# Optimization experiments

Hardware: AMD Instinct MI355X
Metric: run time of the kernel (lower is better)

The kernel has to match this reference:

```python
import jax, jax.numpy as jnp
import numpy as np

N = 131072      # total nodes (1024 graphs x 128 nodes)
E = 1048576     # edges (avg degree 8)
IN = 74         # atom feature length
H = 128         # dim_embedding == all hidden_feats
B = 1024        # batch_size (graphs)
L = 3           # number of GCN+GRU layers


def setup_inputs() -> dict:
    key = jax.random.key(0)
    ks = jax.random.split(key, 10)
    node_feats = jax.random.normal(ks[0], (N, IN), dtype=jnp.float32)
    src = jax.random.randint(ks[1], (E,), 0, N, dtype=jnp.int32)
    dst = jax.random.randint(ks[2], (E,), 0, N, dtype=jnp.int32)
    s_in = 1.0 / np.sqrt(IN)
    s_h = 1.0 / np.sqrt(H)
    # init_transform: Linear(IN, H, bias=False); padding=True zeros the last output unit
    W_init = jax.random.normal(ks[3], (IN, H), dtype=jnp.float32) * s_in
    W_init = W_init.at[:, -1].set(0.0)
    lin_W = jax.random.normal(ks[4], (L, H, H), dtype=jnp.float32) * s_h
    lin_b = jax.random.normal(ks[5], (L, H), dtype=jnp.float32) * s_h
    gru_Wih = jax.random.normal(ks[6], (L, 3 * H, H), dtype=jnp.float32) * s_h
    gru_Whh = jax.random.normal(ks[7], (L, 3 * H, H), dtype=jnp.float32) * s_h
    gru_bih = jax.random.normal(ks[8], (L, 3 * H), dtype=jnp.float32) * s_h
    gru_bhh = jax.random.normal(ks[9], (L, 3 * H), dtype=jnp.float32) * s_h
    return {
        "node_feats": node_feats, "src": src, "dst": dst,
        "W_init": W_init, "lin_W": lin_W, "lin_b": lin_b,
        "gru_Wih": gru_Wih, "gru_Whh": gru_Whh,
        "gru_bih": gru_bih, "gru_bhh": gru_bhh,
        "batch_size": B,
    }


def _gru_cell(x, h, Wih, Whh, bih, bhh):
    # PyTorch GRUCell semantics
    gi = x @ Wih.T + bih   # [N, 3H]
    gh = h @ Whh.T + bhh   # [N, 3H]
    i_r, i_z, i_n = jnp.split(gi, 3, axis=-1)
    h_r, h_z, h_n = jnp.split(gh, 3, axis=-1)
    r = jax.nn.sigmoid(i_r + h_r)
    z = jax.nn.sigmoid(i_z + h_z)
    n = jnp.tanh(i_n + r * h_n)
    return (1.0 - z) * n + z * h


def reference(node_feats, src, dst, W_init, lin_W, lin_b,
              gru_Wih, gru_Whh, gru_bih, gru_bhh, batch_size):
    n_nodes = node_feats.shape[0]
    h = node_feats @ W_init  # init_transform (no bias)
    for l in range(lin_W.shape[0]):
        # update_all: sum incoming source features (scatter-add over edges)
        agg = jax.ops.segment_sum(h[src], dst, num_segments=n_nodes)
        x = jax.nn.relu(agg @ lin_W[l].T + lin_b[l])
        h = _gru_cell(x, h, gru_Wih[l], gru_Whh[l], gru_bih[l], gru_bhh[l])
    return h.reshape(batch_size, -1, h.shape[-1])
```

## Files before the change

### kernel.cpp

```cpp
#include <hip/hip_runtime.h>
#include <hip/hip_bf16.h>

#define NN 131072
#define EE 1048576
#define IN_F 74
#define HH 128
#define LL 3

using f32x4  = __attribute__((ext_vector_type(4))) float;
using f32x16 = __attribute__((ext_vector_type(16))) float;
using bf16x8 = __attribute__((ext_vector_type(8))) short;
typedef unsigned short ushort_t;
typedef unsigned int uint_t;

__device__ __forceinline__ short f2bf(float f) {
    __hip_bfloat16 b = __float2bfloat16(f);
    return __builtin_bit_cast(short, b);
}
__device__ __forceinline__ float bf2f(short s) {
    unsigned int u = ((unsigned int)(unsigned short)s) << 16;
    return __builtin_bit_cast(float, u);
}
__device__ __forceinline__ float bitf(uint_t u) { return __builtin_bit_cast(float, u); }
__device__ __forceinline__ float sigmoidf_(float x) { return 1.f / (1.f + __expf(-x)); }
__device__ __forceinline__ float tanhf_(float x)
{
    x = fminf(fmaxf(x, -15.f), 15.f);
    float e2 = __expf(2.f * x);
    return (e2 - 1.f) / (e2 + 1.f);
}

__global__ __launch_bounds__(256) void k_init_gemm(
    const float* __restrict__ nf, const float* __restrict__ Wi,
    ushort_t* __restrict__ hhi, ushort_t* __restrict__ hlo)
{
    __shared__ float Wis[IN_F * HH];
    __shared__ float nfs[32 * IN_F];
    int b = blockIdx.x;
    int t = threadIdx.x;

    for (int i = t; i < IN_F * HH / 4; i += 256)
        reinterpret_cast<float4*>(Wis)[i] = reinterpret_cast<const float4*>(Wi)[i];
    {
        const float4* nf4 = reinterpret_cast<const float4*>(nf + (long)b * 32 * IN_F);
        for (int i = t; i < 32 * IN_F / 4; i += 256)
            reinterpret_cast<float4*>(nfs)[i] = nf4[i];
    }
    __syncthreads();

    int nl = t >> 3;
    int c0 = (t & 7) * 4;
    float acc[4][4];
#pragma unroll
    for (int hf = 0; hf < 4; ++hf)
#pragma unroll
        for (int j = 0; j < 4; ++j) acc[hf][j] = 0.f;

    const float* nrow = nfs + nl * IN_F;
#pragma unroll 2
    for (int k = 0; k < IN_F; ++k) {
        float a = nrow[k];
#pragma unroll
        for (int hf = 0; hf < 4; ++hf) {
            float4 wv = *reinterpret_cast<const float4*>(Wis + k * HH + hf * 32 + c0);
            acc[hf][0] += a * wv.x;
            acc[hf][1] += a * wv.y;
            acc[hf][2] += a * wv.z;
            acc[hf][3] += a * wv.w;
        }
    }

    int node = b * 32 + nl;
#pragma unroll
    for (int hf = 0; hf < 4; ++hf) {
        uint_t uh[2], ul[2];
#pragma unroll
        for (int p = 0; p < 2; ++p) {
            float v0 = acc[hf][p * 2], v1 = acc[hf][p * 2 + 1];
            short h0 = f2bf(v0), h1 = f2bf(v1);
            short l0 = f2bf(v0 - bf2f(h0)), l1 = f2bf(v1 - bf2f(h1));
            uh[p] = (uint_t)(ushort_t)h0 | ((uint_t)(ushort_t)h1 << 16);
            ul[p] = (uint_t)(ushort_t)l0 | ((uint_t)(ushort_t)l1 << 16);
        }
        long adr = (long)node * HH + hf * 32 + c0;
        *reinterpret_cast<uint2*>(hhi + adr) = make_uint2(uh[0], uh[1]);
        *reinterpret_cast<uint2*>(hlo + adr) = make_uint2(ul[0], ul[1]);
    }
}

__global__ __launch_bounds__(256) void k_hist(const int* __restrict__ dsti, int* __restrict__ deg)
{
    int e = blockIdx.x * 256 + threadIdx.x;
    atomicAdd(&deg[dsti[e]], 1);
}

__global__ __launch_bounds__(256) void k_scan1(const int* __restrict__ deg, int* __restrict__ bsum)
{
    __shared__ int s[256];
    int b = blockIdx.x, t = threadIdx.x;
    int v = 0;
#pragma unroll
    for (int i = 0; i < 4; ++i) v += deg[b * 1024 + t * 4 + i];
    s[t] = v;
    __syncthreads();
    for (int st = 128; st > 0; st >>= 1) {
        if (t < st) s[t] += s[t + st];
        __syncthreads();
    }
    if (t == 0) bsum[b] = s[0];
}

__global__ void k_scan2(int* __restrict__ bsum, int nb)
{
    if (threadIdx.x == 0) {
        int run = 0;
        for (int i = 0; i < nb; ++i) { int v = bsum[i]; bsum[i] = run; run += v; }
    }
}

__global__ __launch_bounds__(256) void k_scan3(
    const int* __restrict__ deg, const int* __restrict__ bsum, int* __restrict__ row_start)
{
    __shared__ int s[256];
    int b = blockIdx.x, t = threadIdx.x;
    int base = b * 1024 + t * 4;
    int d0 = deg[base], d1 = deg[base + 1], d2 = deg[base + 2], d3 = deg[base + 3];
    int local = d0 + d1 + d2 + d3;
    s[t] = local;
    __syncthreads();
    for (int st = 1; st < 256; st <<= 1) {
        int v = (t >= st) ? s[t - st] : 0;
        __syncthreads();
        s[t] += v;
        __syncthreads();
    }
    int excl = s[t] - local + bsum[b];
    row_start[base] = excl;
    row_start[base + 1] = excl + d0;
    row_start[base + 2] = excl + d0 + d1;
    row_start[base + 3] = excl + d0 + d1 + d2;
    if (b == gridDim.x - 1 && t == 255) row_start[NN] = excl + local;
}

__global__ __launch_bounds__(256) void k_fill(
    const int* __restrict__ src, const int* __restrict__ dsti,
    const int* __restrict__ row_start, int* __restrict__ cursor, int* __restrict__ csr_src)
{
    int e = blockIdx.x * 256 + threadIdx.x;
    int d = dsti[e];
    int pos = atomicAdd(&cursor[d], 1);
    csr_src[row_start[d] + pos] = src[e];
}

__global__ __launch_bounds__(256) void k_split(
    const float* __restrict__ srcw, ushort_t* __restrict__ hi,
    ushort_t* __restrict__ lo, int n)
{
    int i = blockIdx.x * 256 + threadIdx.x;
    if (i >= n) return;
    float a = srcw[i];
    short h = f2bf(a);
    float rem = a - bf2f(h);
    hi[i] = (ushort_t)h;
    lo[i] = (ushort_t)f2bf(rem);
}

#define EIDX_CAP 1024

template <bool LDSIDX>
__device__ __forceinline__ void gather_node(
    const ushort_t* __restrict__ plane, const int* __restrict__ eidx,
    const int* __restrict__ csr_src, int estart, int e0, int e1, int c4,
    float& a0, float& a1, float& a2, float& a3)
{
    int e = e0;
    for (; e + 7 < e1; e += 8) {
        uint2 v[8];
#pragma unroll
        for (int u = 0; u < 8; ++u) {
            int s = LDSIDX ? eidx[e + u] : csr_src[estart + e + u];
            v[u] = *reinterpret_cast<const uint2*>(plane + (long)s * HH + c4);
        }
#pragma unroll
        for (int u = 0; u < 8; ++u) {
            a0 += bitf(v[u].x << 16);
            a1 += bitf(v[u].x & 0xffff0000u);
            a2 += bitf(v[u].y << 16);
            a3 += bitf(v[u].y & 0xffff0000u);
        }
    }
    for (; e < e1; ++e) {
        int s = LDSIDX ? eidx[e] : csr_src[estart + e];
        uint2 vv = *reinterpret_cast<const uint2*>(plane + (long)s * HH + c4);
        a0 += bitf(vv.x << 16);
        a1 += bitf(vv.x & 0xffff0000u);
        a2 += bitf(vv.y << 16);
        a3 += bitf(vv.y & 0xffff0000u);
    }
}

__global__ __launch_bounds__(256) void k_x(
    const ushort_t* __restrict__ hhi, const ushort_t* __restrict__ hlo,
    const int* __restrict__ row_start, const int* __restrict__ csr_src,
    const ushort_t* __restrict__ lWhi, const ushort_t* __restrict__ lWlo,
    const float* __restrict__ lb,
    ushort_t* __restrict__ xhi, ushort_t* __restrict__ xlo)
{
    __shared__ float aggs[32 * 128];
    __shared__ int eidx[EIDX_CAP];
    char* abase = (char*)aggs;
    int n0 = blockIdx.x * 32;
    int t = threadIdx.x;
    int w = t >> 6, lane = t & 63;

    int estart = row_start[n0];
    int ecount = row_start[n0 + 32] - estart;
    bool inl = (ecount <= EIDX_CAP);
    for (int i = t; i < ecount && i < EIDX_CAP; i += 256)
        eidx[i] = csr_src[estart + i];
    __syncthreads();

    const ushort_t* plane = (lane >= 32) ? hlo : hhi;
    int c4 = (lane & 31) * 4;

    for (int i = 0; i < 8; ++i) {
        int nl = w * 8 + i;
        int node = n0 + nl;
        int e0 = row_start[node] - estart;
        int e1 = row_start[node + 1] - estart;
        float a0 = 0.f, a1 = 0.f, a2 = 0.f, a3 = 0.f;
        if (inl)
            gather_node<true>(plane, eidx, csr_src, estart, e0, e1, c4, a0, a1, a2, a3);
        else
            gather_node<false>(plane, eidx, csr_src, estart, e0, e1, c4, a0, a1, a2, a3);
        a0 += __shfl_xor(a0, 32, 64);
        a1 += __shfl_xor(a1, 32, 64);
        a2 += __shfl_xor(a2, 32, 64);
        a3 += __shfl_xor(a3, 32, 64);
        if (lane < 32) {
            int swz = (nl & 7) << 4;
            float4 st = make_float4(a0, a1, a2, a3);
            *reinterpret_cast<float4*>(abase + ((nl * 512 + c4 * 4) ^ swz)) = st;
        }
    }
    __syncthreads();

    int ng = w >> 1, jg = w & 1;
    int l16 = lane & 15, lq = lane >> 4;

    f32x4 acc[4];
#pragma unroll
    for (int js = 0; js < 4; ++js) acc[js] = (f32x4){0.f, 0.f, 0.f, 0.f};

#pragma unroll
    for (int kk = 0; kk < 4; ++kk) {
        int k0 = kk * 32;
        int nodeL = ng * 16 + l16;
        int kb = (k0 + lq * 8) * 4;
        int swz = (nodeL & 7) << 4;
        float4 f0 = *reinterpret_cast<const float4*>(abase + ((nodeL * 512 + kb) ^ swz));
        float4 f1 = *reinterpret_cast<const float4*>(abase + ((nodeL * 512 + kb + 16) ^ swz));
        float av[8] = {f0.x, f0.y, f0.z, f0.w, f1.x, f1.y, f1.z, f1.w};
        bf16x8 ahi, alo;
#pragma unroll
        for (int e = 0; e < 8; ++e) {
            short hh_ = f2bf(av[e]);
            ahi[e] = hh_;
            alo[e] = f2bf(av[e] - bf2f(hh_));
        }
#pragma unroll
        for (int js = 0; js < 4; ++js) {
            int jrow = jg * 64 + js * 16 + l16;
            bf16x8 Bh = *reinterpret_cast<const bf16x8*>(lWhi + (long)jrow * HH + k0 + lq * 8);
            bf16x8 Bl = *reinterpret_cast<const bf16x8*>(lWlo + (long)jrow * HH + k0 + lq * 8);
            acc[js] = __builtin_amdgcn_mfma_f32_16x16x32_bf16(ahi, Bh, acc[js], 0, 0, 0);
            acc[js] = __builtin_amdgcn_mfma_f32_16x16x32_bf16(ahi, Bl, acc[js], 0, 0, 0);
            acc[js] = __builtin_amdgcn_mfma_f32_16x16x32_bf16(alo, Bh, acc[js], 0, 0, 0);
        }
    }

#pragma unroll
    for (int js = 0; js < 4; ++js) {
        int j = jg * 64 + js * 16 + l16;
        float bj = lb[j];
#pragma unroll
        for (int r = 0; r < 4; ++r) {
            int node = n0 + ng * 16 + lq * 4 + r;
            float v = fmaxf(acc[js][r] + bj, 0.f);
            long adr = (long)node * HH + j;
            short hi_ = f2bf(v);
            xhi[adr] = (ushort_t)hi_;
            xlo[adr] = (ushort_t)f2bf(v - bf2f(hi_));
        }
    }
}

#define LDSA(p) ((p) * 16384)
#define LDSB(p) (65536 + (p) * 32768)

__device__ __forceinline__ void stage_slab(
    const ushort_t* __restrict__ g, char* lds, int tid, int nchunk512)
{
    const uint4* g4 = reinterpret_cast<const uint4*>(g);
#pragma unroll
    for (int i = 0; i < 4; ++i) {
        if (i >= nchunk512) break;
        int c = i * 512 + tid;
        int L = c * 16;
        int row = L >> 8, kb = L & 255;
        *reinterpret_cast<uint4*>(lds + row * 256 + (kb ^ ((row & 15) << 4))) = g4[c];
    }
}

__device__ __forceinline__ void gru_half(
    f32x16& acc, const char* smem, int pAhi, int myoff, int rs_my,
    int jjoff, int rs_jj, int lh)
{
    bf16x8 Ahi[8], Alo[8];
#pragma unroll
    for (int kc = 0; kc < 8; ++kc) {
        int kb = kc * 32 + lh * 16;
        Ahi[kc] = *reinterpret_cast<const bf16x8*>(smem + LDSA(pAhi)     + myoff + (kb ^ rs_my));
        Alo[kc] = *reinterpret_cast<const bf16x8*>(smem + LDSA(pAhi + 1) + myoff + (kb ^ rs_my));
    }
#pragma unroll
    for (int kc = 0; kc < 8; ++kc) {
        int kb = kc * 32 + lh * 16;
        bf16x8 wh = *reinterpret_cast<const bf16x8*>(smem + LDSB(0) + jjoff + (kb ^ rs_jj));
        bf16x8 wl = *reinterpret_cast<const bf16x8*>(smem + LDSB(1) + jjoff + (kb ^ rs_jj));
        acc = __builtin_amdgcn_mfma_f32_32x32x16_bf16(Ahi[kc], wh, acc, 0, 0, 0);
        acc = __builtin_amdgcn_mfma_f32_32x32x16_bf16(Ahi[kc], wl, acc, 0, 0, 0);
        acc = __builtin_amdgcn_mfma_f32_32x32x16_bf16(Alo[kc], wh, acc, 0, 0, 0);
    }
}

__global__ void k_gru(
    const ushort_t* __restrict__ xhi, const ushort_t* __restrict__ xlo,
    ushort_t* __restrict__ hhi, ushort_t* __restrict__ hlo,
    const ushort_t* __restrict__ Wihhi, const ushort_t* __restrict__ Wihlo,
    const ushort_t* __restrict__ Whhhi, const ushort_t* __restrict__ Whhlo,
    const float* __restrict__ bi, const float* __restrict__ bh)
{
    __shared__ uint4 smem4[131072 / 16];
    char* smem = (char*)smem4;

    int t = threadIdx.x;
    int w = t >> 6, lane = t & 63;
    int ng = w >> 2, og = w & 3;
    int l31 = lane & 31, lh = lane >> 5;
    int n0 = blockIdx.x * 64;
    int myrow = ng * 32 + l31;
    int jj = og * 32 + l31;
    int myoff = myrow * 256, rs_my = (myrow & 15) << 4;
    int jjoff = jj * 256,   rs_jj = (jj & 15) << 4;

    stage_slab(xhi + (long)n0 * HH, smem + LDSA(0), t, 2);
    stage_slab(xlo + (long)n0 * HH, smem + LDSA(1), t, 2);
    stage_slab(hhi + (long)n0 * HH, smem + LDSA(2), t, 2);
    stage_slab(hlo + (long)n0 * HH, smem + LDSA(3), t, 2);
    stage_slab(Whhhi + 256 * HH, smem + LDSB(0), t, 4);
    stage_slab(Whhlo + 256 * HH, smem + LDSB(1), t, 4);
    __syncthreads();

    f32x16 acc1;
#pragma unroll
    for (int i = 0; i < 16; ++i) acc1[i] = 0.f;
    gru_half(acc1, smem, 2, myoff, rs_my, jjoff, rs_jj, lh);

    f32x16 acc2;
#pragma unroll
    for (int i = 0; i < 16; ++i) acc2[i] = 0.f;
    __syncthreads();
    stage_slab(Wihhi, smem + LDSB(0), t, 4);
    stage_slab(Wihlo, smem + LDSB(1), t, 4);
    __syncthreads();
    gru_half(acc2, smem, 0, myoff, rs_my, jjoff, rs_jj, lh);
    __syncthreads();
    stage_slab(Whhhi, smem + LDSB(0), t, 4);
    stage_slab(Whhlo, smem + LDSB(1), t, 4);
    __syncthreads();
    gru_half(acc2, smem, 2, myoff, rs_my, jjoff, rs_jj, lh);
    {
        float bR = bi[jj] + bh[jj];
        float bNh = bh[256 + jj];
#pragma unroll
        for (int i = 0; i < 16; ++i)
            acc1[i] = sigmoidf_(acc2[i] + bR) * (acc1[i] + bNh);
    }

#pragma unroll
    for (int i = 0; i < 16; ++i) acc2[i] = 0.f;
    __syncthreads();
    stage_slab(Wihhi + 256 * HH, smem + LDSB(0), t, 4);
    stage_slab(Wihlo + 256 * HH, smem + LDSB(1), t, 4);
    __syncthreads();
    gru_half(acc2, smem, 0, myoff, rs_my, jjoff, rs_jj, lh);
    {
        float bNi = bi[256 + jj];
#pragma unroll
        for (int i = 0; i < 16; ++i)
            acc1[i] = tanhf_(acc2[i] + bNi + acc1[i]);
    }

#pragma unroll
    for (int i = 0; i < 16; ++i) acc2[i] = 0.f;
    __syncthreads();
    stage_slab(Wihhi + 128 * HH, smem + LDSB(0), t, 4);
    stage_slab(Wihlo + 128 * HH, smem + LDSB(1), t, 4);
    __syncthreads();
    gru_half(acc2, smem, 0, myoff, rs_my, jjoff, rs_jj, lh);
    __syncthreads();
    stage_slab(Whhhi + 128 * HH, smem + LDSB(0), t, 4);
    stage_slab(Whhlo + 128 * HH, smem + LDSB(1), t, 4);
    __syncthreads();
    gru_half(acc2, smem, 2, myoff, rs_my, jjoff, rs_jj, lh);

    {
        float bZ = bi[128 + jj] + bh[128 + jj];
        int kb2 = 2 * jj;
#pragma unroll
        for (int reg = 0; reg < 16; ++reg) {
            int ndl = ng * 32 + (reg & 3) + 8 * (reg >> 2) + 4 * lh;
            long adr = (long)(n0 + ndl) * HH + jj;
            int rsn = (ndl & 15) << 4;
            float hold = bf2f(*reinterpret_cast<const short*>(smem + LDSA(2) + ndl * 256 + (kb2 ^ rsn)))
                       + bf2f(*reinterpret_cast<const short*>(smem + LDSA(3) + ndl * 256 + (kb2 ^ rsn)));
            float zv = sigmoidf_(acc2[reg] + bZ);
            float hp = (1.f - zv) * acc1[reg] + zv * hold;
            short hi_ = f2bf(hp);
            hhi[adr] = (ushort_t)hi_;
            hlo[adr] = (ushort_t)f2bf(hp - bf2f(hi_));
        }
    }
}

__global__ __launch_bounds__(256) void k_copy(
    const uint_t* __restrict__ hhi, const uint_t* __restrict__ hlo,
    float2* __restrict__ out)
{
    long i = (long)blockIdx.x * 256 + threadIdx.x;
    uint_t vh = hhi[i], vl = hlo[i];
    float2 o;
    o.x = bitf(vh << 16) + bitf(vl << 16);
    o.y = bitf(vh & 0xffff0000u) + bitf(vl & 0xffff0000u);
    out[i] = o;
}

extern "C" void kernel_launch(void* const* d_in, const int* in_sizes, int n_in,
                              void* d_out, int out_size, void* d_ws, size_t ws_size,
                              hipStream_t stream)
{
    const float* nf     = (const float*)d_in[0];
    const int*   src    = (const int*)d_in[1];
    const int*   dsti   = (const int*)d_in[2];
    const float* W_init = (const float*)d_in[3];
    const float* lin_W  = (const float*)d_in[4];
    const float* lin_b  = (const float*)d_in[5];
    const float* Wih    = (const float*)d_in[6];
    const float* Whh    = (const float*)d_in[7];
    const float* bih    = (const float*)d_in[8];
    const float* bhh    = (const float*)d_in[9];

    char* ws = (char*)d_ws;
    ushort_t* hhi = (ushort_t*)ws;
    ushort_t* hlo = (ushort_t*)(ws + (32ull << 20));
    ushort_t* xhi = (ushort_t*)(ws + (64ull << 20));
    ushort_t* xlo = (ushort_t*)(ws + (96ull << 20));
    int* deg    = (int*)(ws + (64ull << 20));
    int* cursor = (int*)(ws + (64ull << 20) + (1 << 20));
    int* bsum   = (int*)(ws + (64ull << 20) + (2 << 20));

    char* ob = (char*)d_out;
    int* row_start = (int*)ob;
    int* csr_src   = (int*)(ob + (1ull << 20));
    ushort_t* lWhi  = (ushort_t*)(ob + (6ull << 20));
    ushort_t* lWlo  = lWhi  + 3 * 128 * 128;
    ushort_t* Wihhi = lWlo  + 3 * 128 * 128;
    ushort_t* Wihlo = Wihhi + 3 * 384 * 128;
    ushort_t* Whhhi = Wihlo + 3 * 384 * 128;
    ushort_t* Whhlo = Whhhi + 3 * 384 * 128;

    k_init_gemm<<<NN / 32, 256, 0, stream>>>(nf, W_init, hhi, hlo);

    hipMemsetAsync(deg, 0, (size_t)NN * 4, stream);
    hipMemsetAsync(cursor, 0, (size_t)NN * 4, stream);
    k_hist<<<EE / 256, 256, 0, stream>>>(dsti, deg);
    k_scan1<<<NN / 1024, 256, 0, stream>>>(deg, bsum);
    k_scan2<<<1, 64, 0, stream>>>(bsum, NN / 1024);
    k_scan3<<<NN / 1024, 256, 0, stream>>>(deg, bsum, row_start);
    k_fill<<<EE / 256, 256, 0, stream>>>(src, dsti, row_start, cursor, csr_src);

    k_split<<<(3 * 128 * 128 + 255) / 256, 256, 0, stream>>>(lin_W, lWhi, lWlo, 3 * 128 * 128);
    k_split<<<(3 * 384 * 128 + 255) / 256, 256, 0, stream>>>(Wih, Wihhi, Wihlo, 3 * 384 * 128);
    k_split<<<(3 * 384 * 128 + 255) / 256, 256, 0, stream>>>(Whh, Whhhi, Whhlo, 3 * 384 * 128);

    for (int l = 0; l < LL; ++l) {
        k_x<<<NN / 32, 256, 0, stream>>>(
            hhi, hlo, row_start, csr_src,
            lWhi + (long)l * 128 * 128, lWlo + (long)l * 128 * 128,
            lin_b + (long)l * 128, xhi, xlo);
        k_gru<<<NN / 64, 512, 0, stream>>>(
            xhi, xlo, hhi, hlo,
            Wihhi + (long)l * 384 * 128, Wihlo + (long)l * 384 * 128,
            Whhhi + (long)l * 384 * 128, Whhlo + (long)l * 384 * 128,
            bih + (long)l * 384, bhh + (long)l * 384);
    }

    k_copy<<<NN * HH / 2 / 256, 256, 0, stream>>>((const uint_t*)hhi, (const uint_t*)hlo, (float2*)d_out);
}
```

Baseline: 972.9 us.

## Interleave h hi/lo planes per node and double-buffer GRU weight slabs

The hidden state is stored as one interleaved buffer (hi and lo bf16 halves adjacent per node), so each gathered source row is a single contiguous 512-byte read instead of two separate 256-byte reads from distinct planes. The GRU kernel is restructured into a 12-step loop over weight slabs that stages hi and lo weights separately into alternating LDS buffers, prefetching the next slab into registers while the current one is consumed. This replaces the serial stage/sync/compute pattern and cuts the LDS weight footprint per step. It adds register pressure for the prefetch and keeps two barriers per step.

```diff
diff --git a/kernel.cpp b/kernel.cpp
--- a/kernel.cpp
+++ b/kernel.cpp
@@ -32,7 +32,7 @@
 
 __global__ __launch_bounds__(256) void k_init_gemm(
     const float* __restrict__ nf, const float* __restrict__ Wi,
-    ushort_t* __restrict__ hhi, ushort_t* __restrict__ hlo)
+    ushort_t* __restrict__ h2)
 {
     __shared__ float Wis[IN_F * HH];
     __shared__ float nfs[32 * IN_F];
@@ -82,9 +82,9 @@
             uh[p] = (uint_t)(ushort_t)h0 | ((uint_t)(ushort_t)h1 << 16);
             ul[p] = (uint_t)(ushort_t)l0 | ((uint_t)(ushort_t)l1 << 16);
         }
-        long adr = (long)node * HH + hf * 32 + c0;
-        *reinterpret_cast<uint2*>(hhi + adr) = make_uint2(uh[0], uh[1]);
-        *reinterpret_cast<uint2*>(hlo + adr) = make_uint2(ul[0], ul[1]);
+        long adr = (long)node * 256 + hf * 32 + c0;
+        *reinterpret_cast<uint2*>(h2 + adr) = make_uint2(uh[0], uh[1]);
+        *reinterpret_cast<uint2*>(h2 + adr + 128) = make_uint2(ul[0], ul[1]);
     }
 }
 
@@ -169,8 +169,8 @@
 
 template <bool LDSIDX>
 __device__ __forceinline__ void gather_node(
-    const ushort_t* __restrict__ plane, const int* __restrict__ eidx,
-    const int* __restrict__ csr_src, int estart, int e0, int e1, int c4,
+    const ushort_t* __restrict__ h2, const int* __restrict__ eidx,
+    const int* __restrict__ csr_src, int estart, int e0, int e1, int l4,
     float& a0, float& a1, float& a2, float& a3)
 {
     int e = e0;
@@ -179,7 +179,7 @@
 #pragma unroll
         for (int u = 0; u < 8; ++u) {
             int s = LDSIDX ? eidx[e + u] : csr_src[estart + e + u];
-            v[u] = *reinterpret_cast<const uint2*>(plane + (long)s * HH + c4);
+            v[u] = *reinterpret_cast<const uint2*>(h2 + (long)s * 256 + l4);
         }
 #pragma unroll
         for (int u = 0; u < 8; ++u) {
@@ -191,7 +191,7 @@
     }
     for (; e < e1; ++e) {
         int s = LDSIDX ? eidx[e] : csr_src[estart + e];
-        uint2 vv = *reinterpret_cast<const uint2*>(plane + (long)s * HH + c4);
+        uint2 vv = *reinterpret_cast<const uint2*>(h2 + (long)s * 256 + l4);
         a0 += bitf(vv.x << 16);
         a1 += bitf(vv.x & 0xffff0000u);
         a2 += bitf(vv.y << 16);
@@ -200,7 +200,7 @@
 }
 
 __global__ __launch_bounds__(256) void k_x(
-    const ushort_t* __restrict__ hhi, const ushort_t* __restrict__ hlo,
+    const ushort_t* __restrict__ h2,
     const int* __restrict__ row_start, const int* __restrict__ csr_src,
     const ushort_t* __restrict__ lWhi, const ushort_t* __restrict__ lWlo,
     const float* __restrict__ lb,
@@ -220,8 +220,7 @@
         eidx[i] = csr_src[estart + i];
     __syncthreads();
 
-    const ushort_t* plane = (lane >= 32) ? hlo : hhi;
-    int c4 = (lane & 31) * 4;
+    int l4 = lane * 4;
 
     for (int i = 0; i < 8; ++i) {
         int nl = w * 8 + i;
@@ -230,9 +229,9 @@
         int e1 = row_start[node + 1] - estart;
         float a0 = 0.f, a1 = 0.f, a2 = 0.f, a3 = 0.f;
         if (inl)
-            gather_node<true>(plane, eidx, csr_src, estart, e0, e1, c4, a0, a1, a2, a3);
+            gather_node<true>(h2, eidx, csr_src, estart, e0, e1, l4, a0, a1, a2, a3);
         else
-            gather_node<false>(plane, eidx, csr_src, estart, e0, e1, c4, a0, a1, a2, a3);
+            gather_node<false>(h2, eidx, csr_src, estart, e0, e1, l4, a0, a1, a2, a3);
         a0 += __shfl_xor(a0, 32, 64);
         a1 += __shfl_xor(a1, 32, 64);
         a2 += __shfl_xor(a2, 32, 64);
@@ -240,7 +239,7 @@
         if (lane < 32) {
             int swz = (nl & 7) << 4;
             float4 st = make_float4(a0, a1, a2, a3);
-            *reinterpret_cast<float4*>(abase + ((nl * 512 + c4 * 4) ^ swz)) = st;
+            *reinterpret_cast<float4*>(abase + ((nl * 512 + l4 * 4) ^ swz)) = st;
         }
     }
     __syncthreads();
@@ -295,125 +294,138 @@
     }
 }
 
-#define LDSA(p) ((p) * 16384)
-#define LDSB(p) (65536 + (p) * 32768)
-
-__device__ __forceinline__ void stage_slab(
-    const ushort_t* __restrict__ g, char* lds, int tid, int nchunk512)
-{
-    const uint4* g4 = reinterpret_cast<const uint4*>(g);
-#pragma unroll
-    for (int i = 0; i < 4; ++i) {
-        if (i >= nchunk512) break;
-        int c = i * 512 + tid;
-        int L = c * 16;
-        int row = L >> 8, kb = L & 255;
-        *reinterpret_cast<uint4*>(lds + row * 256 + (kb ^ ((row & 15) << 4))) = g4[c];
-    }
-}
-
-__device__ __forceinline__ void gru_half(
-    f32x16& acc, const char* smem, int pAhi, int myoff, int rs_my,
-    int jjoff, int rs_jj, int lh)
-{
-    bf16x8 Ahi[8], Alo[8];
+#define LDS_XH 0
+#define LDS_XL 16384
+#define LDS_H2 32768
+#define LDS_B0 65536
+#define LDS_B1 98304
+
+__device__ __forceinline__ void slab_mfma(
+    f32x16& acc, const char* pAhi, const char* pAlo, int rs_my,
+    const char* pB, int rs_jj, int lh, bool twoM)
+{
 #pragma unroll
     for (int kc = 0; kc < 8; ++kc) {
         int kb = kc * 32 + lh * 16;
-        Ahi[kc] = *reinterpret_cast<const bf16x8*>(smem + LDSA(pAhi)     + myoff + (kb ^ rs_my));
-        Alo[kc] = *reinterpret_cast<const bf16x8*>(smem + LDSA(pAhi + 1) + myoff + (kb ^ rs_my));
-    }
-#pragma unroll
-    for (int kc = 0; kc < 8; ++kc) {
-        int kb = kc * 32 + lh * 16;
-        bf16x8 wh = *reinterpret_cast<const bf16x8*>(smem + LDSB(0) + jjoff + (kb ^ rs_jj));
-        bf16x8 wl = *reinterpret_cast<const bf16x8*>(smem + LDSB(1) + jjoff + (kb ^ rs_jj));
-        acc = __builtin_amdgcn_mfma_f32_32x32x16_bf16(Ahi[kc], wh, acc, 0, 0, 0);
-        acc = __builtin_amdgcn_mfma_f32_32x32x16_bf16(Ahi[kc], wl, acc, 0, 0, 0);
-        acc = __builtin_amdgcn_mfma_f32_32x32x16_bf16(Alo[kc], wh, acc, 0, 0, 0);
+        bf16x8 a0 = *reinterpret_cast<const bf16x8*>(pAhi + (kb ^ rs_my));
+        bf16x8 bb = *reinterpret_cast<const bf16x8*>(pB + (kb ^ rs_jj));
+        acc = __builtin_amdgcn_mfma_f32_32x32x16_bf16(a0, bb, acc, 0, 0, 0);
+        if (twoM) {
+            bf16x8 a1 = *reinterpret_cast<const bf16x8*>(pAlo + (kb ^ rs_my));
+            acc = __builtin_amdgcn_mfma_f32_32x32x16_bf16(a1, bb, acc, 0, 0, 0);
+        }
     }
 }
 
 __global__ void k_gru(
     const ushort_t* __restrict__ xhi, const ushort_t* __restrict__ xlo,
-    ushort_t* __restrict__ hhi, ushort_t* __restrict__ hlo,
+    ushort_t* __restrict__ h2,
     const ushort_t* __restrict__ Wihhi, const ushort_t* __restrict__ Wihlo,
     const ushort_t* __restrict__ Whhhi, const ushort_t* __restrict__ Whhlo,
     const float* __restrict__ bi, const float* __restrict__ bh)
 {
     __shared__ uint4 smem4[131072 / 16];
     char* smem = (char*)smem4;
-
     int t = threadIdx.x;
     int w = t >> 6, lane = t & 63;
     int ng = w >> 2, og = w & 3;
     int l31 = lane & 31, lh = lane >> 5;
     int n0 = blockIdx.x * 64;
-    int myrow = ng * 32 + l31;
-    int jj = og * 32 + l31;
-    int myoff = myrow * 256, rs_my = (myrow & 15) << 4;
-    int jjoff = jj * 256,   rs_jj = (jj & 15) << 4;
-
-    stage_slab(xhi + (long)n0 * HH, smem + LDSA(0), t, 2);
-    stage_slab(xlo + (long)n0 * HH, smem + LDSA(1), t, 2);
-    stage_slab(hhi + (long)n0 * HH, smem + LDSA(2), t, 2);
-    stage_slab(hlo + (long)n0 * HH, smem + LDSA(3), t, 2);
-    stage_slab(Whhhi + 256 * HH, smem + LDSB(0), t, 4);
-    stage_slab(Whhlo + 256 * HH, smem + LDSB(1), t, 4);
-    __syncthreads();
-
-    f32x16 acc1;
-#pragma unroll
-    for (int i = 0; i < 16; ++i) acc1[i] = 0.f;
-    gru_half(acc1, smem, 2, myoff, rs_my, jjoff, rs_jj, lh);
-
-    f32x16 acc2;
-#pragma unroll
-    for (int i = 0; i < 16; ++i) acc2[i] = 0.f;
-    __syncthreads();
-    stage_slab(Wihhi, smem + LDSB(0), t, 4);
-    stage_slab(Wihlo, smem + LDSB(1), t, 4);
-    __syncthreads();
-    gru_half(acc2, smem, 0, myoff, rs_my, jjoff, rs_jj, lh);
-    __syncthreads();
-    stage_slab(Whhhi, smem + LDSB(0), t, 4);
-    stage_slab(Whhlo, smem + LDSB(1), t, 4);
-    __syncthreads();
-    gru_half(acc2, smem, 2, myoff, rs_my, jjoff, rs_jj, lh);
+    int myrow = ng * 32 + l31, jj = og * 32 + l31;
+    int rs_my = (myrow & 15) << 4, rs_jj = (jj & 15) << 4;
+
+    const ushort_t* wsrc[12] = {
+        Whhhi + 256 * HH, Whhlo + 256 * HH,
+        Wihhi,            Wihlo,
+        Whhhi,            Whhlo,
+        Wihhi + 256 * HH, Wihlo + 256 * HH,
+        Wihhi + 128 * HH, Wihlo + 128 * HH,
+        Whhhi + 128 * HH, Whhlo + 128 * HH };
+    const bool aH[12] = {1, 1, 0, 0, 1, 1, 0, 0, 0, 0, 1, 1};
+
+    uint4 p0, p1, p2, p3;
     {
-        float bR = bi[jj] + bh[jj];
-        float bNh = bh[256 + jj];
-#pragma unroll
-        for (int i = 0; i < 16; ++i)
-            acc1[i] = sigmoidf_(acc2[i] + bR) * (acc1[i] + bNh);
-    }
-
-#pragma unroll
-    for (int i = 0; i < 16; ++i) acc2[i] = 0.f;
-    __syncthreads();
-    stage_slab(Wihhi + 256 * HH, smem + LDSB(0), t, 4);
-    stage_slab(Wihlo + 256 * HH, smem + LDSB(1), t, 4);
-    __syncthreads();
-    gru_half(acc2, smem, 0, myoff, rs_my, jjoff, rs_jj, lh);
+        const uint4* g = reinterpret_cast<const uint4*>(wsrc[0]);
+        p0 = g[t]; p1 = g[512 + t]; p2 = g[1024 + t]; p3 = g[1536 + t];
+    }
     {
-        float bNi = bi[256 + jj];
-#pragma unroll
-        for (int i = 0; i < 16; ++i)
-            acc1[i] = tanhf_(acc2[i] + bNi + acc1[i]);
-    }
-
-#pragma unroll
-    for (int i = 0; i < 16; ++i) acc2[i] = 0.f;
-    __syncthreads();
-    stage_slab(Wihhi + 128 * HH, smem + LDSB(0), t, 4);
-    stage_slab(Wihlo + 128 * HH, smem + LDSB(1), t, 4);
-    __syncthreads();
-    gru_half(acc2, smem, 0, myoff, rs_my, jjoff, rs_jj, lh);
-    __syncthreads();
-    stage_slab(Whhhi + 128 * HH, smem + LDSB(0), t, 4);
-    stage_slab(Whhlo + 128 * HH, smem + LDSB(1), t, 4);
-    __syncthreads();
-    gru_half(acc2, smem, 2, myoff, rs_my, jjoff, rs_jj, lh);
+        const uint4* gxh = reinterpret_cast<const uint4*>(xhi + (long)n0 * HH);
+        const uint4* gxl = reinterpret_cast<const uint4*>(xlo + (long)n0 * HH);
+        const uint4* gh  = reinterpret_cast<const uint4*>(h2 + (long)n0 * 256);
+        uint4 xa = gxh[t], xb = gxh[512 + t];
+        uint4 la = gxl[t], lb2 = gxl[512 + t];
+        uint4 ha = gh[t], hb = gh[512 + t], hc = gh[1024 + t], hd = gh[1536 + t];
+        int c, row, bo;
+        c = t;       row = c >> 4; bo = (c & 15) * 16;
+        *(uint4*)(smem + LDS_XH + row * 256 + (bo ^ ((row & 15) << 4))) = xa;
+        *(uint4*)(smem + LDS_XL + row * 256 + (bo ^ ((row & 15) << 4))) = la;
+        c = 512 + t; row = c >> 4; bo = (c & 15) * 16;
+        *(uint4*)(smem + LDS_XH + row * 256 + (bo ^ ((row & 15) << 4))) = xb;
+        *(uint4*)(smem + LDS_XL + row * 256 + (bo ^ ((row & 15) << 4))) = lb2;
+        c = t;        row = c >> 5; bo = (c & 31) * 16;
+        *(uint4*)(smem + LDS_H2 + row * 512 + (bo & 256) + ((bo & 255) ^ ((row & 15) << 4))) = ha;
+        c = 512 + t;  row = c >> 5; bo = (c & 31) * 16;
+        *(uint4*)(smem + LDS_H2 + row * 512 + (bo & 256) + ((bo & 255) ^ ((row & 15) << 4))) = hb;
+        c = 1024 + t; row = c >> 5; bo = (c & 31) * 16;
+        *(uint4*)(smem + LDS_H2 + row * 512 + (bo & 256) + ((bo & 255) ^ ((row & 15) << 4))) = hc;
+        c = 1536 + t; row = c >> 5; bo = (c & 31) * 16;
+        *(uint4*)(smem + LDS_H2 + row * 512 + (bo & 256) + ((bo & 255) ^ ((row & 15) << 4))) = hd;
+    }
+
+    f32x16 acc1, acc2;
+#pragma unroll
+    for (int i = 0; i < 16; ++i) { acc1[i] = 0.f; acc2[i] = 0.f; }
+
+#pragma unroll
+    for (int s = 0; s < 12; ++s) {
+        int bufbase = (s & 1) ? LDS_B1 : LDS_B0;
+        {
+            int c, row, bo;
+            c = t;        row = c >> 4; bo = (c & 15) * 16;
+            *(uint4*)(smem + bufbase + row * 256 + (bo ^ ((row & 15) << 4))) = p0;
+            c = 512 + t;  row = c >> 4; bo = (c & 15) * 16;
+            *(uint4*)(smem + bufbase + row * 256 + (bo ^ ((row & 15) << 4))) = p1;
+            c = 1024 + t; row = c >> 4; bo = (c & 15) * 16;
+            *(uint4*)(smem + bufbase + row * 256 + (bo ^ ((row & 15) << 4))) = p2;
+            c = 1536 + t; row = c >> 4; bo = (c & 15) * 16;
+            *(uint4*)(smem + bufbase + row * 256 + (bo ^ ((row & 15) << 4))) = p3;
+        }
+        if (s < 11) {
+            const uint4* g = reinterpret_cast<const uint4*>(wsrc[s + 1]);
+            p0 = g[t]; p1 = g[512 + t]; p2 = g[1024 + t]; p3 = g[1536 + t];
+        }
+        __syncthreads();
+        {
+            const char* pA  = aH[s] ? (smem + LDS_H2 + myrow * 512)
+                                    : (smem + LDS_XH + myrow * 256);
+            const char* pAl = aH[s] ? (smem + LDS_H2 + myrow * 512 + 256)
+                                    : (smem + LDS_XL + myrow * 256);
+            const char* pB  = smem + bufbase + jj * 256;
+            bool twoM = (s & 1) == 0;
+            if (s < 2)
+                slab_mfma(acc1, pA, pAl, rs_my, pB, rs_jj, lh, twoM);
+            else
+                slab_mfma(acc2, pA, pAl, rs_my, pB, rs_jj, lh, twoM);
+        }
+        if (s == 5) {
+            float bR = bi[jj] + bh[jj];
+            float bNh = bh[256 + jj];
+#pragma unroll
+            for (int i = 0; i < 16; ++i) {
+                acc1[i] = sigmoidf_(acc2[i] + bR) * (acc1[i] + bNh);
+                acc2[i] = 0.f;
+            }
+        }
+        if (s == 7) {
+            float bNi = bi[256 + jj];
+#pragma unroll
+            for (int i = 0; i < 16; ++i) {
+                acc1[i] = tanhf_(acc2[i] + bNi + acc1[i]);
+                acc2[i] = 0.f;
+            }
+        }
+        __syncthreads();
+    }
 
     {
         float bZ = bi[128 + jj] + bh[128 + jj];
@@ -421,25 +433,26 @@
 #pragma unroll
         for (int reg = 0; reg < 16; ++reg) {
             int ndl = ng * 32 + (reg & 3) + 8 * (reg >> 2) + 4 * lh;
-            long adr = (long)(n0 + ndl) * HH + jj;
             int rsn = (ndl & 15) << 4;
-            float hold = bf2f(*reinterpret_cast<const short*>(smem + LDSA(2) + ndl * 256 + (kb2 ^ rsn)))
-                       + bf2f(*reinterpret_cast<const short*>(smem + LDSA(3) + ndl * 256 + (kb2 ^ rsn)));
+            float hold = bf2f(*reinterpret_cast<const short*>(smem + LDS_H2 + ndl * 512 + (kb2 ^ rsn)))
+                       + bf2f(*reinterpret_cast<const short*>(smem + LDS_H2 + ndl * 512 + 256 + (kb2 ^ rsn)));
             float zv = sigmoidf_(acc2[reg] + bZ);
             float hp = (1.f - zv) * acc1[reg] + zv * hold;
+            long adr = (long)(n0 + ndl) * 256 + jj;
             short hi_ = f2bf(hp);
-            hhi[adr] = (ushort_t)hi_;
-            hlo[adr] = (ushort_t)f2bf(hp - bf2f(hi_));
+            h2[adr] = (ushort_t)hi_;
+            h2[adr + 128] = (ushort_t)f2bf(hp - bf2f(hi_));
         }
     }
 }
 
 __global__ __launch_bounds__(256) void k_copy(
-    const uint_t* __restrict__ hhi, const uint_t* __restrict__ hlo,
-    float2* __restrict__ out)
+    const ushort_t* __restrict__ h2, float2* __restrict__ out)
 {
     long i = (long)blockIdx.x * 256 + threadIdx.x;
-    uint_t vh = hhi[i], vl = hlo[i];
+    int node = (int)(i >> 6), cp = (int)(i & 63);
+    uint_t vh = *reinterpret_cast<const uint_t*>(h2 + (long)node * 256 + cp * 2);
+    uint_t vl = *reinterpret_cast<const uint_t*>(h2 + (long)node * 256 + 128 + cp * 2);
     float2 o;
     o.x = bitf(vh << 16) + bitf(vl << 16);
     o.y = bitf(vh & 0xffff0000u) + bitf(vl & 0xffff0000u);
@@ -462,8 +475,7 @@
     const float* bhh    = (const float*)d_in[9];
 
     char* ws = (char*)d_ws;
-    ushort_t* hhi = (ushort_t*)ws;
-    ushort_t* hlo = (ushort_t*)(ws + (32ull << 20));
+    ushort_t* h2  = (ushort_t*)ws;
     ushort_t* xhi = (ushort_t*)(ws + (64ull << 20));
     ushort_t* xlo = (ushort_t*)(ws + (96ull << 20));
     int* deg    = (int*)(ws + (64ull << 20));
@@ -480,7 +492,7 @@
     ushort_t* Whhhi = Wihlo + 3 * 384 * 128;
     ushort_t* Whhlo = Whhhi + 3 * 384 * 128;
 
-    k_init_gemm<<<NN / 32, 256, 0, stream>>>(nf, W_init, hhi, hlo);
+    k_init_gemm<<<NN / 32, 256, 0, stream>>>(nf, W_init, h2);
 
     hipMemsetAsync(deg, 0, (size_t)NN * 4, stream);
     hipMemsetAsync(cursor, 0, (size_t)NN * 4, stream);
@@ -496,15 +508,15 @@
 
     for (int l = 0; l < LL; ++l) {
         k_x<<<NN / 32, 256, 0, stream>>>(
-            hhi, hlo, row_start, csr_src,
+            h2, row_start, csr_src,
             lWhi + (long)l * 128 * 128, lWlo + (long)l * 128 * 128,
             lin_b + (long)l * 128, xhi, xlo);
         k_gru<<<NN / 64, 512, 0, stream>>>(
-            xhi, xlo, hhi, hlo,
+            xhi, xlo, h2,
             Wihhi + (long)l * 384 * 128, Wihlo + (long)l * 384 * 128,
             Whhhi + (long)l * 384 * 128, Whhlo + (long)l * 384 * 128,
             bih + (long)l * 384, bhh + (long)l * 384);
     }
 
-    k_copy<<<NN * HH / 2 / 256, 256, 0, stream>>>((const uint_t*)hhi, (const uint_t*)hlo, (float2*)d_out);
-}
+    k_copy<<<NN * 64 / 256, 256, 0, stream>>>(h2, (float2*)d_out);
+}
```

Measured after the change: 1.055 ms. 8.4% more time.
